# Optimization experiments

Hardware: AMD Instinct MI355X
Metric: run time of the kernel (lower is better)

The kernel has to match this reference:

```python
import jax, jax.numpy as jnp
import numpy as np

B, T, D, H, L = 64, 512, 1024, 1024, 4


def setup_inputs() -> dict:
    key = jax.random.key(0)
    ks = jax.random.split(key, 7)
    s = 1.0 / np.sqrt(H)
    x = jax.random.normal(ks[0], (B, T, D), dtype=jnp.float32)
    dt = jax.random.uniform(ks[1], (B, T), dtype=jnp.float32)  # positive time deltas
    W_ih = jax.random.uniform(ks[2], (L, 3 * H, D), minval=-s, maxval=s, dtype=jnp.float32)
    W_hh = jax.random.uniform(ks[3], (L, 3 * H, H), minval=-s, maxval=s, dtype=jnp.float32)
    b_ih = jax.random.uniform(ks[4], (L, 3 * H), minval=-s, maxval=s, dtype=jnp.float32)
    b_hh = jax.random.uniform(ks[5], (L, 3 * H), minval=-s, maxval=s, dtype=jnp.float32)
    tau = jax.random.uniform(ks[6], (L, H), minval=0.5, maxval=2.0, dtype=jnp.float32)
    return {"x": x, "dt": dt, "W_ih": W_ih, "W_hh": W_hh, "b_ih": b_ih, "b_hh": b_hh, "tau": tau}


def reference(x, dt, W_ih, W_hh, b_ih, b_hh, tau):
    # x: [B,T,D], dt: [B,T]; stacked per-layer params: W_ih [L,3H,D], W_hh [L,3H,H],
    # b_ih/b_hh [L,3H], tau [L,H] (learned time constants, 'exp' scaling).
    n_layers = W_hh.shape[0]
    hid = W_hh.shape[2]
    inv_tau = 1.0 / jax.nn.softplus(tau)  # [L,H]

    def step(h, xt):
        # h: [B,L,H]; x_t: [B,D]; dt_t: [B]
        x_t, dt_t = xt
        inp = x_t
        new_h = []
        for i in range(n_layers):  # fixed small layer count
            decay = jnp.exp(-dt_t[:, None] * inv_tau[i])        # [B,H] exp time scaling
            hd = h[:, i] * decay
            gx = inp @ W_ih[i].T + b_ih[i]                       # [B,3H]
            gh = hd @ W_hh[i].T + b_hh[i]                        # [B,3H]
            xr, xz, xn = jnp.split(gx, 3, axis=-1)
            hr, hz, hn = jnp.split(gh, 3, axis=-1)
            r = jax.nn.sigmoid(xr + hr)
            z = jax.nn.sigmoid(xz + hz)
            n = jnp.tanh(xn + r * hn)
            h_i = (1.0 - z) * n + z * hd                         # torch GRU convention
            new_h.append(h_i)
            inp = h_i
        return jnp.stack(new_h, axis=1), new_h[-1]

    h0 = jnp.zeros((x.shape[0], n_layers, hid), dtype=x.dtype)
    xs = (jnp.swapaxes(x, 0, 1), jnp.swapaxes(dt, 0, 1))  # time-major for scan
    _, seq = jax.lax.scan(step, h0, xs)                    # seq: [T,B,H]
    return jnp.swapaxes(seq, 0, 1)                         # [B,T,H]
```

## Files before the change

### kernel.cpp

```cpp
#include <hip/hip_runtime.h>

typedef _Float16 f16;
typedef _Float16 half8 __attribute__((ext_vector_type(8)));
typedef float f32x4 __attribute__((ext_vector_type(4)));
typedef float f32x2 __attribute__((ext_vector_type(2)));

#define TT 512
#define HID 1024

__device__ __forceinline__ half8 cvt8(f32x4 lo, f32x4 hi) {
  half8 r;
  r[0]=(f16)lo[0]; r[1]=(f16)lo[1]; r[2]=(f16)lo[2]; r[3]=(f16)lo[3];
  r[4]=(f16)hi[0]; r[5]=(f16)hi[1]; r[6]=(f16)hi[2]; r[7]=(f16)hi[3];
  return r;
}
__device__ __forceinline__ void st_sc_u32(unsigned* p, unsigned v) {
  asm volatile("global_store_dword %0, %1, off sc0 sc1" :: "v"(p), "v"(v) : "memory");
}
__device__ __forceinline__ unsigned ld_sc_u32(const unsigned* p) {
  unsigned v;
  asm volatile("global_load_dword %0, %1, off sc0 sc1\n\ts_waitcnt vmcnt(0)"
               : "=v"(v) : "v"(p) : "memory");
  return v;
}
__device__ __forceinline__ void spinFlag(const unsigned* p) {
  int gd = 0;
  while (ld_sc_u32(p) == 0u) { __builtin_amdgcn_s_sleep(1); if (++gd > (1<<20)) break; }
}
__device__ __forceinline__ float sigm(float x)  { return 1.f/(1.f + __expf(-x)); }
__device__ __forceinline__ float ftanh(float x) { return 1.f - 2.f/(1.f + __expf(2.f*x)); }

__global__ void init_misc(const float* __restrict__ x, f16* __restrict__ xh) {
  size_t idx = (size_t)blockIdx.x*256 + threadIdx.x;
  size_t i = idx*8;
  int d = (int)(i & 1023);
  size_t bt = i >> 10;
  int t = (int)(bt & 511), b = (int)(bt >> 9);
  f32x4 a = *(const f32x4*)(x+i);
  f32x4 c4 = *(const f32x4*)(x+i+4);
  int s = d >> 4, c = d & 15;
  *(half8*)(xh + (((size_t)t*64 + s)*64 + b)*16 + c) = cvt8(a,c4);
}

__global__ __launch_bounds__(512, 2) void tsgru_k(
    const float* __restrict__ dtp, const float* __restrict__ Wih,
    const float* __restrict__ Whh, const float* __restrict__ bih,
    const float* __restrict__ bhh, const float* __restrict__ tau,
    const f16* __restrict__ xh, f16* __restrict__ H, f16* __restrict__ HD,
    unsigned* __restrict__ flags, float* __restrict__ out) {
  extern __shared__ char lds[];
  float* PART = (float*)lds;

  const int tid = threadIdx.x, lane = tid & 63, wv = tid >> 6;
  const int wg = blockIdx.x, layer = wg >> 6, wgl = wg & 63, col0 = wgl*16;
  const int u = (lane >> 4) & 3;

  const float* WihL = Wih + (size_t)layer*3072*HID;
  const float* WhhL = Whh + (size_t)layer*3072*HID;
  const int wcol = col0 + (lane & 15);
  half8 bW[2][3][4];
  #pragma unroll
  for (int g=0;g<2;g++)
    #pragma unroll
    for (int q=0;q<3;q++)
      #pragma unroll
      for (int ks=0;ks<4;ks++) {
        const float* p = (g ? WhhL : WihL) + (size_t)(q*HID + wcol)*HID + wv*128 + ks*32 + u*8;
        bW[g][q][ks] = cvt8(*(const f32x4*)p, *(const f32x4*)(p+4));
      }

  const int gb = tid >> 3, gc2 = (tid & 7)*2;
  float biR[2],biZ[2],biN[2],bhR[2],bhZ[2],bhN[2],ni[2];
  #pragma unroll
  for (int e=0;e<2;e++) {
    const int c = col0 + gc2 + e;
    biR[e]=bih[layer*3072+c]; biZ[e]=bih[layer*3072+1024+c]; biN[e]=bih[layer*3072+2048+c];
    bhR[e]=bhh[layer*3072+c]; bhZ[e]=bhh[layer*3072+1024+c]; bhN[e]=bhh[layer*3072+2048+c];
    ni[e] = -1.0f / log1pf(expf(tau[layer*HID + c]));
  }

  const int baseA = (wv*8 + (u>>1))*1024 + (lane&15)*16 + (u&1)*8;

  const f16* gxBase = (layer==0) ? xh : H + (size_t)(layer-1)*TT*65536;
  f16* HDl = HD + (size_t)layer*32*65536;
  unsigned* flagOwn = flags + (size_t)layer*TT*64;
  const unsigned* flagUp = flags + (size_t)(layer>0 ? layer-1 : 0)*TT*64;

  float hdv0 = 0.f, hdv1 = 0.f;

  for (int t = 0; t < TT; ++t) {
    const float dtg1 = (t < TT-1) ? dtp[gb*TT + t + 1] : 0.f;

    if (layer > 0 && wv == 0) spinFlag(flagUp + (size_t)t*64 + lane);
    __builtin_amdgcn_s_barrier();

    const f16* gxP = gxBase + (size_t)t*65536;
    half8 aF[2][4];
    #pragma unroll
    for (int ks=0;ks<2;ks++)
      #pragma unroll
      for (int m=0;m<4;m++)
        aF[ks][m] = *(const half8*)(gxP + baseA + ks*2048 + m*256);

    f32x4 acc[4][3];
    #pragma unroll
    for (int m=0;m<4;m++) { acc[m][0]=(f32x4){0.f,0.f,0.f,0.f}; acc[m][1]=acc[m][0]; acc[m][2]=acc[m][0]; }
    #pragma unroll
    for (int ks=0;ks<4;ks++) {
      #pragma unroll
      for (int m=0;m<4;m++) {
        const half8 a = aF[ks&1][m];
        acc[m][0] = __builtin_amdgcn_mfma_f32_16x16x32_f16(a, bW[0][0][ks], acc[m][0],0,0,0);
        acc[m][1] = __builtin_amdgcn_mfma_f32_16x16x32_f16(a, bW[0][1][ks], acc[m][1],0,0,0);
        acc[m][2] = __builtin_amdgcn_mfma_f32_16x16x32_f16(a, bW[0][2][ks], acc[m][2],0,0,0);
      }
      if (ks<2) {
        #pragma unroll
        for (int m=0;m<4;m++)
          aF[ks&1][m] = *(const half8*)(gxP + baseA + (ks+2)*2048 + m*256);
      }
    }
    {
      float* Pb = PART + (size_t)(wv*3)*1088 + (lane&15)*68 + u*4;
      #pragma unroll
      for (int q=0;q<3;q++)
        #pragma unroll
        for (int m=0;m<4;m++)
          *(f32x4*)(Pb + q*1088 + m*16) = acc[m][q];
    }
    asm volatile("s_waitcnt lgkmcnt(0)" ::: "memory");
    __builtin_amdgcn_s_barrier();

    float sx0[2]={0.f,0.f}, sx1[2]={0.f,0.f}, sx2[2]={0.f,0.f};
    #pragma unroll
    for (int e=0;e<2;e++) {
      const int pb = (gc2+e)*68 + gb;
      #pragma unroll
      for (int w8=0;w8<8;w8++) {
        const float* P = PART + (size_t)(w8*3)*1088 + pb;
        sx0[e] += P[0]; sx1[e] += P[1088]; sx2[e] += P[2176];
      }
    }

    if (t > 0 && lane != wgl) spinFlag(flagOwn + (size_t)(t-1)*64 + lane);
    const f16* ghP = HDl + (size_t)(t & 31)*65536;
    if (t > 0) {
      #pragma unroll
      for (int ks=0;ks<2;ks++)
        #pragma unroll
        for (int m=0;m<4;m++)
          aF[ks][m] = *(const half8*)(ghP + baseA + ks*2048 + m*256);
    }
    asm volatile("s_waitcnt lgkmcnt(0)" ::: "memory");
    __builtin_amdgcn_s_barrier();

    #pragma unroll
    for (int m=0;m<4;m++) { acc[m][0]=(f32x4){0.f,0.f,0.f,0.f}; acc[m][1]=acc[m][0]; acc[m][2]=acc[m][0]; }
    if (t > 0) {
      #pragma unroll
      for (int ks=0;ks<4;ks++) {
        #pragma unroll
        for (int m=0;m<4;m++) {
          const half8 a = aF[ks&1][m];
          acc[m][0] = __builtin_amdgcn_mfma_f32_16x16x32_f16(a, bW[1][0][ks], acc[m][0],0,0,0);
          acc[m][1] = __builtin_amdgcn_mfma_f32_16x16x32_f16(a, bW[1][1][ks], acc[m][1],0,0,0);
          acc[m][2] = __builtin_amdgcn_mfma_f32_16x16x32_f16(a, bW[1][2][ks], acc[m][2],0,0,0);
        }
        if (ks<2) {
          #pragma unroll
          for (int m=0;m<4;m++)
            aF[ks&1][m] = *(const half8*)(ghP + baseA + (ks+2)*2048 + m*256);
        }
      }
    }
    {
      float* Pb = PART + (size_t)(wv*3)*1088 + (lane&15)*68 + u*4;
      #pragma unroll
      for (int q=0;q<3;q++)
        #pragma unroll
        for (int m=0;m<4;m++)
          *(f32x4*)(Pb + q*1088 + m*16) = acc[m][q];
    }
    asm volatile("s_waitcnt lgkmcnt(0)" ::: "memory");
    __builtin_amdgcn_s_barrier();

    {
      float hv[2];
      #pragma unroll
      for (int e=0;e<2;e++) {
        const int pb = (gc2+e)*68 + gb;
        float sh0=0.f, sh1=0.f, sh2=0.f;
        #pragma unroll
        for (int w8=0;w8<8;w8++) {
          const float* P = PART + (size_t)(w8*3)*1088 + pb;
          sh0 += P[0]; sh1 += P[1088]; sh2 += P[2176];
        }
        const float hdv = e ? hdv1 : hdv0;
        const float r = sigm(sx0[e] + biR[e] + sh0 + bhR[e]);
        const float z = sigm(sx1[e] + biZ[e] + sh1 + bhZ[e]);
        const float n = ftanh(sx2[e] + biN[e] + r*(sh2 + bhN[e]));
        hv[e] = (1.f - z)*n + z*hdv;
      }
      union { f16 h[2]; unsigned uu; } pk;
      const size_t slot = (size_t)(wgl*64 + gb)*16 + gc2;
      if (layer < 3) {
        pk.h[0]=(f16)hv[0]; pk.h[1]=(f16)hv[1];
        st_sc_u32((unsigned*)(H + ((size_t)layer*TT + t)*65536 + slot), pk.uu);
      } else {
        f32x2 v; v[0]=hv[0]; v[1]=hv[1];
        *(f32x2*)(out + ((size_t)gb*TT + t)*HID + col0 + gc2) = v;
      }
      if (t < TT-1) {
        const float hd0 = hv[0]*__expf(dtg1*ni[0]);
        const float hd1 = hv[1]*__expf(dtg1*ni[1]);
        pk.h[0]=(f16)hd0; pk.h[1]=(f16)hd1;
        st_sc_u32((unsigned*)(HDl + (size_t)((t+1)&31)*65536 + slot), pk.uu);
        hdv0 = hd0; hdv1 = hd1;
      }
    }
    asm volatile("s_waitcnt vmcnt(0) lgkmcnt(0)" ::: "memory");
    __builtin_amdgcn_s_barrier();
    if (tid == 0) st_sc_u32(flagOwn + (size_t)t*64 + wgl, 1u);
  }
}

extern "C" void kernel_launch(void* const* d_in, const int* in_sizes, int n_in,
                              void* d_out, int out_size, void* d_ws, size_t ws_size,
                              hipStream_t stream) {
  const float* x   = (const float*)d_in[0];
  const float* dtp = (const float*)d_in[1];
  const float* Wih = (const float*)d_in[2];
  const float* Whh = (const float*)d_in[3];
  const float* bih = (const float*)d_in[4];
  const float* bhh = (const float*)d_in[5];
  const float* tau = (const float*)d_in[6];
  float* out = (float*)d_out;
  char* ws = (char*)d_ws;

  f16* xh = (f16*)ws;
  f16* H  = (f16*)(ws + 67108864);
  f16* HD = (f16*)(ws + 268435456);
  unsigned* flags = (unsigned*)(ws + 268435456 + 16777216);

  (void)hipMemsetAsync(flags, 0, 524288, stream);
  init_misc<<<16384, 256, 0, stream>>>(x, xh);
  const int ldsBytes = 104448;
  (void)hipFuncSetAttribute((const void*)tsgru_k, hipFuncAttributeMaxDynamicSharedMemorySize, ldsBytes);
  tsgru_k<<<256, 512, ldsBytes, stream>>>(dtp, Wih, Whh, bih, bhh, tau, xh, H, HD, flags, out);
}
```

Baseline: 5.055 ms.

## Merge input and hidden GEMMs into one phase with per-wave atomic flags

Both polls (upstream-layer flag and own-layer previous-step flag) now happen before a single barrier. The input and recurrent MFMA passes then run back to back, sharing accumulators for the r/z gates and keeping the n-gate hidden part separate, which removes one LDS reduction and two block barriers per step. Per-workgroup completion flags become counters: each wave atomically increments after its stores, and readers wait until all 8 waves have reported, so the end-of-step barrier is gone. Blocks are remapped so layers interleave across block IDs, biases are staged in LDS, and the LDS footprint grows, which may reduce occupancy.

New measurement: 7.206 ms. +42.5%, slower.

```diff
diff --git a/kernel.cpp b/kernel.cpp
--- a/kernel.cpp
+++ b/kernel.cpp
@@ -23,9 +23,9 @@
                : "=v"(v) : "v"(p) : "memory");
   return v;
 }
-__device__ __forceinline__ void spinFlag(const unsigned* p) {
-  int gd = 0;
-  while (ld_sc_u32(p) == 0u) { __builtin_amdgcn_s_sleep(1); if (++gd > (1<<20)) break; }
+__device__ __forceinline__ void atom_inc_sc(unsigned* p) {
+  unsigned one = 1u;
+  asm volatile("global_atomic_add %0, %1, off sc1" :: "v"(p), "v"(one) : "memory");
 }
 __device__ __forceinline__ float sigm(float x)  { return 1.f/(1.f + __expf(-x)); }
 __device__ __forceinline__ float ftanh(float x) { return 1.f - 2.f/(1.f + __expf(2.f*x)); }
@@ -49,10 +49,14 @@
     const f16* __restrict__ xh, f16* __restrict__ H, f16* __restrict__ HD,
     unsigned* __restrict__ flags, float* __restrict__ out) {
   extern __shared__ char lds[];
-  float* PART = (float*)lds;
+  float* PART  = (float*)lds;
+  float* biasS = (float*)(lds + 139264);
 
   const int tid = threadIdx.x, lane = tid & 63, wv = tid >> 6;
-  const int wg = blockIdx.x, layer = wg >> 6, wgl = wg & 63, col0 = wgl*16;
+  const int bid = blockIdx.x;
+  const int layer = (bid & 7) >> 1;
+  const int wgl = (bid >> 3) | ((bid & 1) << 5);
+  const int col0 = wgl * 16;
   const int u = (lane >> 4) & 3;
 
   const float* WihL = Wih + (size_t)layer*3072*HID;
@@ -69,18 +73,17 @@
         bW[g][q][ks] = cvt8(*(const f32x4*)p, *(const f32x4*)(p+4));
       }
 
+  if (tid < 96) {
+    int j = tid >> 4, c = tid & 15;
+    biasS[tid] = (j < 3) ? bih[layer*3072 + j*HID + col0 + c]
+                         : bhh[layer*3072 + (j-3)*HID + col0 + c];
+  }
   const int gb = tid >> 3, gc2 = (tid & 7)*2;
-  float biR[2],biZ[2],biN[2],bhR[2],bhZ[2],bhN[2],ni[2];
-  #pragma unroll
-  for (int e=0;e<2;e++) {
-    const int c = col0 + gc2 + e;
-    biR[e]=bih[layer*3072+c]; biZ[e]=bih[layer*3072+1024+c]; biN[e]=bih[layer*3072+2048+c];
-    bhR[e]=bhh[layer*3072+c]; bhZ[e]=bhh[layer*3072+1024+c]; bhN[e]=bhh[layer*3072+2048+c];
-    ni[e] = -1.0f / log1pf(expf(tau[layer*HID + c]));
-  }
+  const float ni0 = -1.f/log1pf(expf(tau[layer*HID + col0 + gc2]));
+  const float ni1 = -1.f/log1pf(expf(tau[layer*HID + col0 + gc2 + 1]));
+  __syncthreads();
 
   const int baseA = (wv*8 + (u>>1))*1024 + (lane&15)*16 + (u&1)*8;
-
   const f16* gxBase = (layer==0) ? xh : H + (size_t)(layer-1)*TT*65536;
   f16* HDl = HD + (size_t)layer*32*65536;
   unsigned* flagOwn = flags + (size_t)layer*TT*64;
@@ -91,114 +94,99 @@
   for (int t = 0; t < TT; ++t) {
     const float dtg1 = (t < TT-1) ? dtp[gb*TT + t + 1] : 0.f;
 
-    if (layer > 0 && wv == 0) spinFlag(flagUp + (size_t)t*64 + lane);
+    if (wv == 0 && layer > 0) {
+      int gd = 0;
+      while (!__all(ld_sc_u32(flagUp + (size_t)t*64 + lane) >= 8u)) { if (++gd > (1<<20)) break; }
+    }
+    if (wv == 1 && t > 0) {
+      int gd = 0;
+      while (!__all(ld_sc_u32(flagOwn + (size_t)(t-1)*64 + lane) >= 8u)) { if (++gd > (1<<20)) break; }
+    }
     __builtin_amdgcn_s_barrier();
 
     const f16* gxP = gxBase + (size_t)t*65536;
-    half8 aF[2][4];
+    const f16* ghP = HDl + (size_t)(t & 31)*65536;
+
+    half8 ax[2][4], ah[2][4];
     #pragma unroll
     for (int ks=0;ks<2;ks++)
       #pragma unroll
       for (int m=0;m<4;m++)
-        aF[ks][m] = *(const half8*)(gxP + baseA + ks*2048 + m*256);
-
-    f32x4 acc[4][3];
-    #pragma unroll
-    for (int m=0;m<4;m++) { acc[m][0]=(f32x4){0.f,0.f,0.f,0.f}; acc[m][1]=acc[m][0]; acc[m][2]=acc[m][0]; }
+        ax[ks][m] = *(const half8*)(gxP + baseA + ks*2048 + m*256);
+    if (t > 0) {
+      #pragma unroll
+      for (int ks=0;ks<2;ks++)
+        #pragma unroll
+        for (int m=0;m<4;m++)
+          ah[ks][m] = *(const half8*)(ghP + baseA + ks*2048 + m*256);
+    }
+
+    f32x4 acc[4][4];
+    #pragma unroll
+    for (int m=0;m<4;m++) {
+      acc[m][0]=(f32x4){0.f,0.f,0.f,0.f}; acc[m][1]=acc[m][0];
+      acc[m][2]=acc[m][0]; acc[m][3]=acc[m][0];
+    }
+
     #pragma unroll
     for (int ks=0;ks<4;ks++) {
       #pragma unroll
       for (int m=0;m<4;m++) {
-        const half8 a = aF[ks&1][m];
+        const half8 a = ax[ks&1][m];
         acc[m][0] = __builtin_amdgcn_mfma_f32_16x16x32_f16(a, bW[0][0][ks], acc[m][0],0,0,0);
         acc[m][1] = __builtin_amdgcn_mfma_f32_16x16x32_f16(a, bW[0][1][ks], acc[m][1],0,0,0);
         acc[m][2] = __builtin_amdgcn_mfma_f32_16x16x32_f16(a, bW[0][2][ks], acc[m][2],0,0,0);
       }
-      if (ks<2) {
+      if (ks < 2) {
         #pragma unroll
         for (int m=0;m<4;m++)
-          aF[ks&1][m] = *(const half8*)(gxP + baseA + (ks+2)*2048 + m*256);
-      }
-    }
+          ax[ks&1][m] = *(const half8*)(gxP + baseA + (ks+2)*2048 + m*256);
+      }
+    }
+    if (t > 0) {
+      #pragma unroll
+      for (int ks=0;ks<4;ks++) {
+        #pragma unroll
+        for (int m=0;m<4;m++) {
+          const half8 a = ah[ks&1][m];
+          acc[m][0] = __builtin_amdgcn_mfma_f32_16x16x32_f16(a, bW[1][0][ks], acc[m][0],0,0,0);
+          acc[m][1] = __builtin_amdgcn_mfma_f32_16x16x32_f16(a, bW[1][1][ks], acc[m][1],0,0,0);
+          acc[m][3] = __builtin_amdgcn_mfma_f32_16x16x32_f16(a, bW[1][2][ks], acc[m][3],0,0,0);
+        }
+        if (ks < 2) {
+          #pragma unroll
+          for (int m=0;m<4;m++)
+            ah[ks&1][m] = *(const half8*)(ghP + baseA + (ks+2)*2048 + m*256);
+        }
+      }
+    }
+
     {
-      float* Pb = PART + (size_t)(wv*3)*1088 + (lane&15)*68 + u*4;
-      #pragma unroll
-      for (int q=0;q<3;q++)
+      float* Pb = PART + (size_t)(wv*4)*1088 + (lane&15)*68 + u*4;
+      #pragma unroll
+      for (int s=0;s<4;s++)
         #pragma unroll
         for (int m=0;m<4;m++)
-          *(f32x4*)(Pb + q*1088 + m*16) = acc[m][q];
+          *(f32x4*)(Pb + s*1088 + m*16) = acc[m][s];
     }
     asm volatile("s_waitcnt lgkmcnt(0)" ::: "memory");
     __builtin_amdgcn_s_barrier();
 
-    float sx0[2]={0.f,0.f}, sx1[2]={0.f,0.f}, sx2[2]={0.f,0.f};
-    #pragma unroll
-    for (int e=0;e<2;e++) {
-      const int pb = (gc2+e)*68 + gb;
-      #pragma unroll
-      for (int w8=0;w8<8;w8++) {
-        const float* P = PART + (size_t)(w8*3)*1088 + pb;
-        sx0[e] += P[0]; sx1[e] += P[1088]; sx2[e] += P[2176];
-      }
-    }
-
-    if (t > 0 && lane != wgl) spinFlag(flagOwn + (size_t)(t-1)*64 + lane);
-    const f16* ghP = HDl + (size_t)(t & 31)*65536;
-    if (t > 0) {
-      #pragma unroll
-      for (int ks=0;ks<2;ks++)
-        #pragma unroll
-        for (int m=0;m<4;m++)
-          aF[ks][m] = *(const half8*)(ghP + baseA + ks*2048 + m*256);
-    }
-    asm volatile("s_waitcnt lgkmcnt(0)" ::: "memory");
-    __builtin_amdgcn_s_barrier();
-
-    #pragma unroll
-    for (int m=0;m<4;m++) { acc[m][0]=(f32x4){0.f,0.f,0.f,0.f}; acc[m][1]=acc[m][0]; acc[m][2]=acc[m][0]; }
-    if (t > 0) {
-      #pragma unroll
-      for (int ks=0;ks<4;ks++) {
-        #pragma unroll
-        for (int m=0;m<4;m++) {
-          const half8 a = aF[ks&1][m];
-          acc[m][0] = __builtin_amdgcn_mfma_f32_16x16x32_f16(a, bW[1][0][ks], acc[m][0],0,0,0);
-          acc[m][1] = __builtin_amdgcn_mfma_f32_16x16x32_f16(a, bW[1][1][ks], acc[m][1],0,0,0);
-          acc[m][2] = __builtin_amdgcn_mfma_f32_16x16x32_f16(a, bW[1][2][ks], acc[m][2],0,0,0);
-        }
-        if (ks<2) {
-          #pragma unroll
-          for (int m=0;m<4;m++)
-            aF[ks&1][m] = *(const half8*)(ghP + baseA + (ks+2)*2048 + m*256);
-        }
-      }
-    }
-    {
-      float* Pb = PART + (size_t)(wv*3)*1088 + (lane&15)*68 + u*4;
-      #pragma unroll
-      for (int q=0;q<3;q++)
-        #pragma unroll
-        for (int m=0;m<4;m++)
-          *(f32x4*)(Pb + q*1088 + m*16) = acc[m][q];
-    }
-    asm volatile("s_waitcnt lgkmcnt(0)" ::: "memory");
-    __builtin_amdgcn_s_barrier();
-
     {
       float hv[2];
       #pragma unroll
       for (int e=0;e<2;e++) {
         const int pb = (gc2+e)*68 + gb;
-        float sh0=0.f, sh1=0.f, sh2=0.f;
+        float S0=0.f,S1=0.f,S2=0.f,S3=0.f;
         #pragma unroll
         for (int w8=0;w8<8;w8++) {
-          const float* P = PART + (size_t)(w8*3)*1088 + pb;
-          sh0 += P[0]; sh1 += P[1088]; sh2 += P[2176];
+          const float* P = PART + (size_t)(w8*4)*1088 + pb;
+          S0 += P[0]; S1 += P[1088]; S2 += P[2176]; S3 += P[3264];
         }
         const float hdv = e ? hdv1 : hdv0;
-        const float r = sigm(sx0[e] + biR[e] + sh0 + bhR[e]);
-        const float z = sigm(sx1[e] + biZ[e] + sh1 + bhZ[e]);
-        const float n = ftanh(sx2[e] + biN[e] + r*(sh2 + bhN[e]));
+        const float r = sigm(S0 + biasS[gc2+e]    + biasS[48+gc2+e]);
+        const float z = sigm(S1 + biasS[16+gc2+e] + biasS[64+gc2+e]);
+        const float n = ftanh(S2 + biasS[32+gc2+e] + r*(S3 + biasS[80+gc2+e]));
         hv[e] = (1.f - z)*n + z*hdv;
       }
       union { f16 h[2]; unsigned uu; } pk;
@@ -211,16 +199,14 @@
         *(f32x2*)(out + ((size_t)gb*TT + t)*HID + col0 + gc2) = v;
       }
       if (t < TT-1) {
-        const float hd0 = hv[0]*__expf(dtg1*ni[0]);
-        const float hd1 = hv[1]*__expf(dtg1*ni[1]);
-        pk.h[0]=(f16)hd0; pk.h[1]=(f16)hd1;
+        hdv0 = hv[0]*__expf(dtg1*ni0);
+        hdv1 = hv[1]*__expf(dtg1*ni1);
+        pk.h[0]=(f16)hdv0; pk.h[1]=(f16)hdv1;
         st_sc_u32((unsigned*)(HDl + (size_t)((t+1)&31)*65536 + slot), pk.uu);
-        hdv0 = hd0; hdv1 = hd1;
-      }
-    }
-    asm volatile("s_waitcnt vmcnt(0) lgkmcnt(0)" ::: "memory");
-    __builtin_amdgcn_s_barrier();
-    if (tid == 0) st_sc_u32(flagOwn + (size_t)t*64 + wgl, 1u);
+      }
+    }
+    asm volatile("s_waitcnt vmcnt(0)" ::: "memory");
+    if (lane == 0) atom_inc_sc(flagOwn + (size_t)t*64 + wgl);
   }
 }
 
@@ -244,7 +230,7 @@
 
   (void)hipMemsetAsync(flags, 0, 524288, stream);
   init_misc<<<16384, 256, 0, stream>>>(x, xh);
-  const int ldsBytes = 104448;
+  const int ldsBytes = 139648;
   (void)hipFuncSetAttribute((const void*)tsgru_k, hipFuncAttributeMaxDynamicSharedMemorySize, ldsBytes);
   tsgru_k<<<256, 512, ldsBytes, stream>>>(dtp, Wih, Whh, bih, bhh, tau, xh, H, HD, flags, out);
 }
```
